# Performance work log

Measured on AMD Instinct MI355X. Metric: run time of the kernel, lower is better.

## Reference

```python
import jax, jax.numpy as jnp
import numpy as np

B, N, D_IN, D_MID, D_OUT = 512, 8192, 128, 256, 16


def setup_inputs() -> dict:
    key = jax.random.key(0)
    k1, k2, k3, k4, k5 = jax.random.split(key, 5)
    return {
        "x": jax.random.normal(k1, (B, D_IN), dtype=jnp.float32),
        "calc_X": jax.random.normal(k2, (N, D_IN), dtype=jnp.float32),
        "calc_Y": jax.random.normal(k3, (N, D_OUT), dtype=jnp.float32),
        "W1": jax.random.normal(k4, (D_MID, D_IN), dtype=jnp.float32) * (D_IN ** -0.5),
        "W2": jax.random.normal(k5, (D_OUT, D_MID), dtype=jnp.float32) * (D_MID ** -0.5),
        "h": jnp.array([1.5], dtype=jnp.float32),
    }


def _mlp(v, W1, W2):
    # fc2(relu(fc1(v))), both linears bias-free
    return jnp.maximum(v @ W1.T, 0.0) @ W2.T


def reference(x, calc_X, calc_Y, W1, W2, h):
    Zw = _mlp(x, W1, W2)        # [B, D_OUT] queries
    Xw = _mlp(calc_X, W1, W2)   # [N, D_OUT] reference embeddings (batched, no loop)
    # Gaussian kernel weights gauss((Xw_j - Zw)/h): [B, N, D_OUT]
    z = (Xw[None, :, :] - Zw[:, None, :]) / h
    w = jnp.exp(-0.5 * z * z)
    denominator = jnp.sum(w, axis=1)                   # [B, D_OUT]
    numerator = jnp.einsum("bnd,nd->bd", w, calc_Y)    # [B, D_OUT]
    return numerator / denominator
```

## Files before the change

kernel.cpp:

```cpp
#include <hip/hip_runtime.h>

#define D_IN  128
#define D_MID 256
#define D_OUT 16
#define NB    512
#define NN    8192
#define NROWS (NB + NN)
#define RPB   16
#define BT    8
#define NSLICE 8
#define SLICE_N (NN / NSLICE)

#define EW_OFF      0
#define PART_OFF    (NROWS * D_OUT)
#define W1T_OFF     (PART_OFF + 2 * NSLICE * NB * D_OUT)
#define W2T_OFF     (W1T_OFF + D_MID * D_IN)

__global__ __launch_bounds__(256) void transpose_kernel(
    const float* __restrict__ W1, const float* __restrict__ W2,
    float* __restrict__ W1T, float* __restrict__ W2T)
{
    const int tid = blockIdx.x * 256 + threadIdx.x;
    if (tid < 8192) {
        const int k4 = tid >> 8;
        const int j  = tid & 255;
        const float4 v = reinterpret_cast<const float4*>(W1)[(size_t)j * 32 + k4];
        reinterpret_cast<float4*>(W1T)[(size_t)k4 * 256 + j] = v;
    } else {
        const int t2 = tid - 8192;
        const int j4 = t2 >> 4;
        const int d  = t2 & 15;
        const float4 v = reinterpret_cast<const float4*>(W2)[(size_t)d * 64 + j4];
        reinterpret_cast<float4*>(W2T)[(size_t)j4 * 16 + d] = v;
    }
}

__global__ __launch_bounds__(256) void mlp_kernel(
    const float* __restrict__ x, const float* __restrict__ calc_X,
    const float* __restrict__ W1T, const float* __restrict__ W2T,
    const float* __restrict__ hptr, float* __restrict__ Ews)
{
    __shared__ float rows[RPB][132];
    __shared__ float hid[RPB][260];

    const int t = threadIdx.x;
    const int row0 = blockIdx.x * RPB;

#pragma unroll
    for (int i = 0; i < 2; ++i) {
        const int idx = t + 256 * i;
        const int r  = idx >> 5;
        const int k4 = idx & 31;
        const int grow = row0 + r;
        const float* src = (grow < NB) ? (x + (size_t)grow * D_IN)
                                       : (calc_X + (size_t)(grow - NB) * D_IN);
        const float4 v = reinterpret_cast<const float4*>(src)[k4];
        *reinterpret_cast<float4*>(&rows[r][k4 * 4]) = v;
    }
    __syncthreads();

    const int jj = t & 63;
    const int rg = t >> 6;

    {
        float acc[4][4] = {};
        const float4* __restrict__ w1t4 = reinterpret_cast<const float4*>(W1T);
#pragma unroll 2
        for (int k4 = 0; k4 < 32; ++k4) {
            float4 wv[4], av[4];
#pragma unroll
            for (int s = 0; s < 4; ++s)
                wv[s] = w1t4[k4 * 256 + s * 64 + jj];
#pragma unroll
            for (int q = 0; q < 4; ++q)
                av[q] = *reinterpret_cast<const float4*>(&rows[rg * 4 + q][k4 * 4]);
#pragma unroll
            for (int q = 0; q < 4; ++q)
#pragma unroll
                for (int s = 0; s < 4; ++s)
                    acc[q][s] = fmaf(av[q].x, wv[s].x, fmaf(av[q].y, wv[s].y,
                                fmaf(av[q].z, wv[s].z, fmaf(av[q].w, wv[s].w, acc[q][s]))));
        }
#pragma unroll
        for (int q = 0; q < 4; ++q)
#pragma unroll
            for (int s = 0; s < 4; ++s)
                hid[rg * 4 + q][s * 64 + jj] = fmaxf(acc[q][s], 0.f);
    }
    __syncthreads();

    {
        const int r = t >> 4;
        const int d = t & 15;
        const float4* __restrict__ w2t4 = reinterpret_cast<const float4*>(W2T);
        float acc = 0.f;
#pragma unroll 4
        for (int j4 = 0; j4 < 64; ++j4) {
            const float4 wv = w2t4[j4 * 16 + d];
            const float4 hv = *reinterpret_cast<const float4*>(&hid[r][j4 * 4]);
            acc = fmaf(hv.x, wv.x, fmaf(hv.y, wv.y, fmaf(hv.z, wv.z, fmaf(hv.w, wv.w, acc))));
        }
        const float scale = 0.84932180028801904272f / hptr[0];
        Ews[(size_t)(row0 + r) * D_OUT + d] = acc * scale;
    }
}

#define GAUSS(xc, yc, zc, num, den) { \
    const float df_ = (xc) - (zc); \
    const float w_ = __builtin_amdgcn_exp2f(-(df_ * df_)); \
    (den) += w_; (num) = fmaf(w_, (yc), (num)); }

__global__ __launch_bounds__(256) void kde_kernel(
    const float* __restrict__ Ews, const float* __restrict__ Y,
    float* __restrict__ partial)
{
    __shared__ float red[4][4][64];

    const int t     = threadIdx.x;
    const int b0    = blockIdx.x * BT;
    const int slice = blockIdx.y;
    const float* __restrict__ Xws = Ews + (size_t)NB * D_OUT;

    const int dg    = t & 3;
    const int chunk = t >> 2;

    float4 z[BT], num[BT], den[BT];
#pragma unroll
    for (int bt = 0; bt < BT; ++bt) {
        z[bt] = reinterpret_cast<const float4*>(Ews + (size_t)(b0 + bt) * D_OUT)[dg];
        num[bt] = make_float4(0.f, 0.f, 0.f, 0.f);
        den[bt] = make_float4(0.f, 0.f, 0.f, 0.f);
    }

#pragma unroll 2
    for (int i = 0; i < SLICE_N / 64; ++i) {
        const int n = slice * SLICE_N + chunk + 64 * i;
        const float4 xw = reinterpret_cast<const float4*>(Xws + (size_t)n * D_OUT)[dg];
        const float4 y  = reinterpret_cast<const float4*>(Y   + (size_t)n * D_OUT)[dg];
#pragma unroll
        for (int bt = 0; bt < BT; ++bt) {
            GAUSS(xw.x, y.x, z[bt].x, num[bt].x, den[bt].x);
            GAUSS(xw.y, y.y, z[bt].y, num[bt].y, den[bt].y);
            GAUSS(xw.z, y.z, z[bt].z, num[bt].z, den[bt].z);
            GAUSS(xw.w, y.w, z[bt].w, num[bt].w, den[bt].w);
        }
    }

    float vals[64];
#pragma unroll
    for (int bt = 0; bt < BT; ++bt) {
        vals[bt * 4 + 0] = num[bt].x; vals[bt * 4 + 1] = num[bt].y;
        vals[bt * 4 + 2] = num[bt].z; vals[bt * 4 + 3] = num[bt].w;
        vals[32 + bt * 4 + 0] = den[bt].x; vals[32 + bt * 4 + 1] = den[bt].y;
        vals[32 + bt * 4 + 2] = den[bt].z; vals[32 + bt * 4 + 3] = den[bt].w;
    }
#pragma unroll
    for (int m = 4; m <= 32; m <<= 1) {
#pragma unroll
        for (int v = 0; v < 64; ++v)
            vals[v] += __shfl_xor(vals[v], m, 64);
    }

    const int wave = t >> 6;
    const int lane = t & 63;
    if (lane < 4) {
#pragma unroll
        for (int v = 0; v < 64; ++v) red[wave][lane][v] = vals[v];
    }
    __syncthreads();

    if (t < 128) {
        const int b = t >> 4;
        const int d = t & 15;
        float nsum = 0.f, dsum = 0.f;
#pragma unroll
        for (int w = 0; w < 4; ++w) {
            nsum += red[w][d >> 2][b * 4 + (d & 3)];
            dsum += red[w][d >> 2][32 + b * 4 + (d & 3)];
        }
        const size_t idx = (size_t)slice * NB * D_OUT + (size_t)(b0 + b) * D_OUT + d;
        partial[idx] = nsum;
        partial[(size_t)NSLICE * NB * D_OUT + idx] = dsum;
    }
}

__global__ __launch_bounds__(256) void combine_kernel(
    const float* __restrict__ partial, float* __restrict__ out)
{
    const int i = blockIdx.x * 256 + threadIdx.x;
    float nsum = 0.f, dsum = 0.f;
#pragma unroll
    for (int s = 0; s < NSLICE; ++s) {
        nsum += partial[(size_t)s * NB * D_OUT + i];
        dsum += partial[(size_t)(NSLICE + s) * NB * D_OUT + i];
    }
    out[i] = nsum / dsum;
}

extern "C" void kernel_launch(void* const* d_in, const int* in_sizes, int n_in,
                              void* d_out, int out_size, void* d_ws, size_t ws_size,
                              hipStream_t stream) {
    const float* x      = (const float*)d_in[0];
    const float* calc_X = (const float*)d_in[1];
    const float* calc_Y = (const float*)d_in[2];
    const float* W1     = (const float*)d_in[3];
    const float* W2     = (const float*)d_in[4];
    const float* h      = (const float*)d_in[5];

    float* ws      = (float*)d_ws;
    float* Ews     = ws + EW_OFF;
    float* partial = ws + PART_OFF;
    float* W1T     = ws + W1T_OFF;
    float* W2T     = ws + W2T_OFF;
    float* out     = (float*)d_out;

    transpose_kernel<<<dim3(36), dim3(256), 0, stream>>>(W1, W2, W1T, W2T);
    mlp_kernel<<<dim3(NROWS / RPB), dim3(256), 0, stream>>>(x, calc_X, W1T, W2T, h, Ews);
    kde_kernel<<<dim3(NB / BT, NSLICE), dim3(256), 0, stream>>>(Ews, calc_Y, partial);
    combine_kernel<<<dim3(NB * D_OUT / 256), dim3(256), 0, stream>>>(partial, out);
}
```

Measured before the change: 47.99 us.

## Expand Gaussian exponent into precomputed linear terms and retune launch shapes

```diff
diff --git a/kernel.cpp b/kernel.cpp
--- a/kernel.cpp
+++ b/kernel.cpp
@@ -6,15 +6,17 @@
 #define NB    512
 #define NN    8192
 #define NROWS (NB + NN)
-#define RPB   16
+#define RPB   8
 #define BT    8
-#define NSLICE 8
+#define NSLICE 4
 #define SLICE_N (NN / NSLICE)
 
-#define EW_OFF      0
-#define PART_OFF    (NROWS * D_OUT)
-#define W1T_OFF     (PART_OFF + 2 * NSLICE * NB * D_OUT)
-#define W2T_OFF     (W1T_OFF + D_MID * D_IN)
+#define ZQ_OFF    0
+#define TARR_OFF  (NB * D_OUT)
+#define ANEG_OFF  (TARR_OFF + NN * D_OUT)
+#define PART_OFF  (ANEG_OFF + NN * D_OUT)
+#define W1T_OFF   (PART_OFF + 2 * NSLICE * NB * D_OUT)
+#define W2T_OFF   (W1T_OFF + D_MID * D_IN)
 
 __global__ __launch_bounds__(256) void transpose_kernel(
     const float* __restrict__ W1, const float* __restrict__ W2,
@@ -38,7 +40,8 @@
 __global__ __launch_bounds__(256) void mlp_kernel(
     const float* __restrict__ x, const float* __restrict__ calc_X,
     const float* __restrict__ W1T, const float* __restrict__ W2T,
-    const float* __restrict__ hptr, float* __restrict__ Ews)
+    const float* __restrict__ hptr,
+    float* __restrict__ zq, float* __restrict__ tarr, float* __restrict__ aneg)
 {
     __shared__ float rows[RPB][132];
     __shared__ float hid[RPB][260];
@@ -46,11 +49,9 @@
     const int t = threadIdx.x;
     const int row0 = blockIdx.x * RPB;
 
-#pragma unroll
-    for (int i = 0; i < 2; ++i) {
-        const int idx = t + 256 * i;
-        const int r  = idx >> 5;
-        const int k4 = idx & 31;
+    {
+        const int r  = t >> 5;
+        const int k4 = t & 31;
         const int grow = row0 + r;
         const float* src = (grow < NB) ? (x + (size_t)grow * D_IN)
                                        : (calc_X + (size_t)(grow - NB) * D_IN);
@@ -63,63 +64,76 @@
     const int rg = t >> 6;
 
     {
-        float acc[4][4] = {};
+        float acc[2][4] = {};
         const float4* __restrict__ w1t4 = reinterpret_cast<const float4*>(W1T);
 #pragma unroll 2
         for (int k4 = 0; k4 < 32; ++k4) {
-            float4 wv[4], av[4];
+            float4 wv[4], av[2];
 #pragma unroll
             for (int s = 0; s < 4; ++s)
                 wv[s] = w1t4[k4 * 256 + s * 64 + jj];
 #pragma unroll
-            for (int q = 0; q < 4; ++q)
-                av[q] = *reinterpret_cast<const float4*>(&rows[rg * 4 + q][k4 * 4]);
-#pragma unroll
-            for (int q = 0; q < 4; ++q)
+            for (int q = 0; q < 2; ++q)
+                av[q] = *reinterpret_cast<const float4*>(&rows[rg * 2 + q][k4 * 4]);
+#pragma unroll
+            for (int q = 0; q < 2; ++q)
 #pragma unroll
                 for (int s = 0; s < 4; ++s)
                     acc[q][s] = fmaf(av[q].x, wv[s].x, fmaf(av[q].y, wv[s].y,
                                 fmaf(av[q].z, wv[s].z, fmaf(av[q].w, wv[s].w, acc[q][s]))));
         }
 #pragma unroll
-        for (int q = 0; q < 4; ++q)
+        for (int q = 0; q < 2; ++q)
 #pragma unroll
             for (int s = 0; s < 4; ++s)
-                hid[rg * 4 + q][s * 64 + jj] = fmaxf(acc[q][s], 0.f);
+                hid[rg * 2 + q][s * 64 + jj] = fmaxf(acc[q][s], 0.f);
     }
     __syncthreads();
 
     {
-        const int r = t >> 4;
-        const int d = t & 15;
+        const int r    = t >> 5;
+        const int d    = t & 15;
+        const int half = (t >> 4) & 1;
         const float4* __restrict__ w2t4 = reinterpret_cast<const float4*>(W2T);
         float acc = 0.f;
 #pragma unroll 4
-        for (int j4 = 0; j4 < 64; ++j4) {
+        for (int k4 = 0; k4 < 32; ++k4) {
+            const int j4 = half * 32 + k4;
             const float4 wv = w2t4[j4 * 16 + d];
             const float4 hv = *reinterpret_cast<const float4*>(&hid[r][j4 * 4]);
             acc = fmaf(hv.x, wv.x, fmaf(hv.y, wv.y, fmaf(hv.z, wv.z, fmaf(hv.w, wv.w, acc))));
         }
-        const float scale = 0.84932180028801904272f / hptr[0];
-        Ews[(size_t)(row0 + r) * D_OUT + d] = acc * scale;
-    }
-}
-
-#define GAUSS(xc, yc, zc, num, den) { \
-    const float df_ = (xc) - (zc); \
-    const float w_ = __builtin_amdgcn_exp2f(-(df_ * df_)); \
-    (den) += w_; (num) = fmaf(w_, (yc), (num)); }
-
-__global__ __launch_bounds__(256) void kde_kernel(
-    const float* __restrict__ Ews, const float* __restrict__ Y,
+        acc += __shfl_xor(acc, 16, 64);
+        if (half == 0) {
+            const float s  = 0.84932180028801904272f / hptr[0];
+            const float zs = acc * s;
+            const int grow = row0 + r;
+            if (grow < NB) {
+                zq[(size_t)grow * D_OUT + d] = zs;
+            } else {
+                const size_t k = (size_t)(grow - NB) * D_OUT + d;
+                tarr[k] = zs + zs;
+                aneg[k] = -zs * zs;
+            }
+        }
+    }
+}
+
+#define GAUSS(tc, ac, yc, zc, num, den) { \
+    const float e_ = fmaf((tc), (zc), (ac)); \
+    const float u_ = __builtin_amdgcn_exp2f(e_); \
+    (den) += u_; (num) = fmaf(u_, (yc), (num)); }
+
+__global__ __launch_bounds__(512) void kde_kernel(
+    const float* __restrict__ zq, const float* __restrict__ tarr,
+    const float* __restrict__ aneg, const float* __restrict__ Y,
     float* __restrict__ partial)
 {
-    __shared__ float red[4][4][64];
+    __shared__ float red[8][4][64];
 
     const int t     = threadIdx.x;
     const int b0    = blockIdx.x * BT;
     const int slice = blockIdx.y;
-    const float* __restrict__ Xws = Ews + (size_t)NB * D_OUT;
 
     const int dg    = t & 3;
     const int chunk = t >> 2;
@@ -127,22 +141,23 @@
     float4 z[BT], num[BT], den[BT];
 #pragma unroll
     for (int bt = 0; bt < BT; ++bt) {
-        z[bt] = reinterpret_cast<const float4*>(Ews + (size_t)(b0 + bt) * D_OUT)[dg];
+        z[bt] = reinterpret_cast<const float4*>(zq + (size_t)(b0 + bt) * D_OUT)[dg];
         num[bt] = make_float4(0.f, 0.f, 0.f, 0.f);
         den[bt] = make_float4(0.f, 0.f, 0.f, 0.f);
     }
 
 #pragma unroll 2
-    for (int i = 0; i < SLICE_N / 64; ++i) {
-        const int n = slice * SLICE_N + chunk + 64 * i;
-        const float4 xw = reinterpret_cast<const float4*>(Xws + (size_t)n * D_OUT)[dg];
-        const float4 y  = reinterpret_cast<const float4*>(Y   + (size_t)n * D_OUT)[dg];
+    for (int i = 0; i < SLICE_N / 128; ++i) {
+        const int n = slice * SLICE_N + chunk + 128 * i;
+        const float4 tv = reinterpret_cast<const float4*>(tarr)[(size_t)n * 4 + dg];
+        const float4 av = reinterpret_cast<const float4*>(aneg)[(size_t)n * 4 + dg];
+        const float4 yv = reinterpret_cast<const float4*>(Y)[(size_t)n * 4 + dg];
 #pragma unroll
         for (int bt = 0; bt < BT; ++bt) {
-            GAUSS(xw.x, y.x, z[bt].x, num[bt].x, den[bt].x);
-            GAUSS(xw.y, y.y, z[bt].y, num[bt].y, den[bt].y);
-            GAUSS(xw.z, y.z, z[bt].z, num[bt].z, den[bt].z);
-            GAUSS(xw.w, y.w, z[bt].w, num[bt].w, den[bt].w);
+            GAUSS(tv.x, av.x, yv.x, z[bt].x, num[bt].x, den[bt].x);
+            GAUSS(tv.y, av.y, yv.y, z[bt].y, num[bt].y, den[bt].y);
+            GAUSS(tv.z, av.z, yv.z, z[bt].z, num[bt].z, den[bt].z);
+            GAUSS(tv.w, av.w, yv.w, z[bt].w, num[bt].w, den[bt].w);
         }
     }
 
@@ -174,7 +189,7 @@
         const int d = t & 15;
         float nsum = 0.f, dsum = 0.f;
 #pragma unroll
-        for (int w = 0; w < 4; ++w) {
+        for (int w = 0; w < 8; ++w) {
             nsum += red[w][d >> 2][b * 4 + (d & 3)];
             dsum += red[w][d >> 2][32 + b * 4 + (d & 3)];
         }
@@ -208,14 +223,17 @@
     const float* h      = (const float*)d_in[5];
 
     float* ws      = (float*)d_ws;
-    float* Ews     = ws + EW_OFF;
+    float* zq      = ws + ZQ_OFF;
+    float* tarr    = ws + TARR_OFF;
+    float* aneg    = ws + ANEG_OFF;
     float* partial = ws + PART_OFF;
     float* W1T     = ws + W1T_OFF;
     float* W2T     = ws + W2T_OFF;
     float* out     = (float*)d_out;
 
     transpose_kernel<<<dim3(36), dim3(256), 0, stream>>>(W1, W2, W1T, W2T);
-    mlp_kernel<<<dim3(NROWS / RPB), dim3(256), 0, stream>>>(x, calc_X, W1T, W2T, h, Ews);
-    kde_kernel<<<dim3(NB / BT, NSLICE), dim3(256), 0, stream>>>(Ews, calc_Y, partial);
+    mlp_kernel<<<dim3(NROWS / RPB), dim3(256), 0, stream>>>(x, calc_X, W1T, W2T, h,
+                                                            zq, tarr, aneg);
+    kde_kernel<<<dim3(NB / BT, NSLICE), dim3(512), 0, stream>>>(zq, tarr, aneg, calc_Y, partial);
     combine_kernel<<<dim3(NB * D_OUT / 256), dim3(256), 0, stream>>>(partial, out);
 }
```

After: 54.52 us. 1.14x slower.

## Halve MLP rows per block, drop LDS input staging, split fc2 reduction

Applied to the files above, without the earlier changes.

```diff
diff --git a/kernel.cpp b/kernel.cpp
--- a/kernel.cpp
+++ b/kernel.cpp
@@ -6,15 +6,15 @@
 #define NB    512
 #define NN    8192
 #define NROWS (NB + NN)
-#define RPB   16
+#define RPB   8
 #define BT    8
 #define NSLICE 8
 #define SLICE_N (NN / NSLICE)
 
-#define EW_OFF      0
-#define PART_OFF    (NROWS * D_OUT)
-#define W1T_OFF     (PART_OFF + 2 * NSLICE * NB * D_OUT)
-#define W2T_OFF     (W1T_OFF + D_MID * D_IN)
+#define EW_OFF    0
+#define PART_OFF  (NROWS * D_OUT)
+#define W1T_OFF   (PART_OFF + 2 * NSLICE * NB * D_OUT)
+#define W2T_OFF   (W1T_OFF + D_MID * D_IN)
 
 __global__ __launch_bounds__(256) void transpose_kernel(
     const float* __restrict__ W1, const float* __restrict__ W2,
@@ -40,68 +40,67 @@
     const float* __restrict__ W1T, const float* __restrict__ W2T,
     const float* __restrict__ hptr, float* __restrict__ Ews)
 {
-    __shared__ float rows[RPB][132];
     __shared__ float hid[RPB][260];
 
     const int t = threadIdx.x;
     const int row0 = blockIdx.x * RPB;
-
-#pragma unroll
-    for (int i = 0; i < 2; ++i) {
-        const int idx = t + 256 * i;
-        const int r  = idx >> 5;
-        const int k4 = idx & 31;
-        const int grow = row0 + r;
+    const int jj = t & 63;
+    const int rg = t >> 6;
+
+    const float4* rp[2];
+#pragma unroll
+    for (int q = 0; q < 2; ++q) {
+        const int grow = row0 + rg * 2 + q;
         const float* src = (grow < NB) ? (x + (size_t)grow * D_IN)
                                        : (calc_X + (size_t)(grow - NB) * D_IN);
-        const float4 v = reinterpret_cast<const float4*>(src)[k4];
-        *reinterpret_cast<float4*>(&rows[r][k4 * 4]) = v;
-    }
-    __syncthreads();
-
-    const int jj = t & 63;
-    const int rg = t >> 6;
+        rp[q] = reinterpret_cast<const float4*>(src);
+    }
 
     {
-        float acc[4][4] = {};
+        float acc[2][4] = {};
         const float4* __restrict__ w1t4 = reinterpret_cast<const float4*>(W1T);
-#pragma unroll 2
+#pragma unroll 4
         for (int k4 = 0; k4 < 32; ++k4) {
-            float4 wv[4], av[4];
+            float4 wv[4], av[2];
 #pragma unroll
             for (int s = 0; s < 4; ++s)
                 wv[s] = w1t4[k4 * 256 + s * 64 + jj];
 #pragma unroll
-            for (int q = 0; q < 4; ++q)
-                av[q] = *reinterpret_cast<const float4*>(&rows[rg * 4 + q][k4 * 4]);
-#pragma unroll
-            for (int q = 0; q < 4; ++q)
+            for (int q = 0; q < 2; ++q)
+                av[q] = rp[q][k4];
+#pragma unroll
+            for (int q = 0; q < 2; ++q)
 #pragma unroll
                 for (int s = 0; s < 4; ++s)
                     acc[q][s] = fmaf(av[q].x, wv[s].x, fmaf(av[q].y, wv[s].y,
                                 fmaf(av[q].z, wv[s].z, fmaf(av[q].w, wv[s].w, acc[q][s]))));
         }
 #pragma unroll
-        for (int q = 0; q < 4; ++q)
+        for (int q = 0; q < 2; ++q)
 #pragma unroll
             for (int s = 0; s < 4; ++s)
-                hid[rg * 4 + q][s * 64 + jj] = fmaxf(acc[q][s], 0.f);
+                hid[rg * 2 + q][s * 64 + jj] = fmaxf(acc[q][s], 0.f);
     }
     __syncthreads();
 
     {
-        const int r = t >> 4;
-        const int d = t & 15;
+        const int r    = t >> 5;
+        const int d    = t & 15;
+        const int half = (t >> 4) & 1;
         const float4* __restrict__ w2t4 = reinterpret_cast<const float4*>(W2T);
         float acc = 0.f;
 #pragma unroll 4
-        for (int j4 = 0; j4 < 64; ++j4) {
+        for (int k4 = 0; k4 < 32; ++k4) {
+            const int j4 = half * 32 + k4;
             const float4 wv = w2t4[j4 * 16 + d];
             const float4 hv = *reinterpret_cast<const float4*>(&hid[r][j4 * 4]);
             acc = fmaf(hv.x, wv.x, fmaf(hv.y, wv.y, fmaf(hv.z, wv.z, fmaf(hv.w, wv.w, acc))));
         }
-        const float scale = 0.84932180028801904272f / hptr[0];
-        Ews[(size_t)(row0 + r) * D_OUT + d] = acc * scale;
+        acc += __shfl_xor(acc, 16, 64);
+        if (half == 0) {
+            const float s = 0.84932180028801904272f / hptr[0];
+            Ews[(size_t)(row0 + r) * D_OUT + d] = acc * s;
+        }
     }
 }
 
@@ -135,14 +134,14 @@
 #pragma unroll 2
     for (int i = 0; i < SLICE_N / 64; ++i) {
         const int n = slice * SLICE_N + chunk + 64 * i;
-        const float4 xw = reinterpret_cast<const float4*>(Xws + (size_t)n * D_OUT)[dg];
-        const float4 y  = reinterpret_cast<const float4*>(Y   + (size_t)n * D_OUT)[dg];
+        const float4 xw = reinterpret_cast<const float4*>(Xws)[(size_t)n * 4 + dg];
+        const float4 yv = reinterpret_cast<const float4*>(Y)[(size_t)n * 4 + dg];
 #pragma unroll
         for (int bt = 0; bt < BT; ++bt) {
-            GAUSS(xw.x, y.x, z[bt].x, num[bt].x, den[bt].x);
-            GAUSS(xw.y, y.y, z[bt].y, num[bt].y, den[bt].y);
-            GAUSS(xw.z, y.z, z[bt].z, num[bt].z, den[bt].z);
-            GAUSS(xw.w, y.w, z[bt].w, num[bt].w, den[bt].w);
+            GAUSS(xw.x, yv.x, z[bt].x, num[bt].x, den[bt].x);
+            GAUSS(xw.y, yv.y, z[bt].y, num[bt].y, den[bt].y);
+            GAUSS(xw.z, yv.z, z[bt].z, num[bt].z, den[bt].z);
+            GAUSS(xw.w, yv.w, z[bt].w, num[bt].w, den[bt].w);
         }
     }
 
```

Measured after the change: 62.14 us. 1.29x slower.
